# Optimization experiments

Measured on AMD Instinct MI355X. Metric: run time of the kernel, lower is better.

## Reference

```python
import jax, jax.numpy as jnp
import numpy as np

D_MODEL = 1024
NUM_HEADS = 16
HEAD_DIM = D_MODEL // NUM_HEADS  # 64
ROPE_THETA = 10000.0
BATCH = 2
SEQ = 2048
NEG_INF = -1e30


def setup_inputs() -> dict:
    key = jax.random.key(0)
    ks = jax.random.split(key, 6)
    std = 1.0 / np.sqrt(D_MODEL)
    x = jax.random.normal(ks[0], (BATCH, SEQ, D_MODEL), dtype=jnp.float32)
    wq = jax.random.normal(ks[1], (D_MODEL, D_MODEL), dtype=jnp.float32) * std
    wk = jax.random.normal(ks[2], (D_MODEL, D_MODEL), dtype=jnp.float32) * std
    wv = jax.random.normal(ks[3], (D_MODEL, D_MODEL), dtype=jnp.float32) * std
    wo = jax.random.normal(ks[4], (D_MODEL, D_MODEL), dtype=jnp.float32) * std
    token_positions = jnp.broadcast_to(jnp.arange(SEQ, dtype=jnp.int32)[None, :], (BATCH, SEQ))
    return {"x": x, "token_positions": token_positions, "wq": wq, "wk": wk, "wv": wv, "wo": wo}


def _apply_rope(t, token_positions):
    # t: (B, H, S, head_dim), token_positions: (B, S)
    half = HEAD_DIM // 2
    inv_freq = 1.0 / (ROPE_THETA ** (2.0 * jnp.arange(half, dtype=jnp.float32) / HEAD_DIM))
    angles = token_positions.astype(jnp.float32)[..., None] * inv_freq  # (B, S, half)
    cos = jnp.cos(angles)[:, None, :, :]  # (B, 1, S, half)
    sin = jnp.sin(angles)[:, None, :, :]
    tp = t.reshape(*t.shape[:-1], half, 2)  # interleaved pairs
    x1, x2 = tp[..., 0], tp[..., 1]
    r1 = x1 * cos - x2 * sin
    r2 = x1 * sin + x2 * cos
    return jnp.stack([r1, r2], axis=-1).reshape(t.shape)


def reference(x, token_positions, wq, wk, wv, wo):
    B, S, D = x.shape
    H, hd = NUM_HEADS, HEAD_DIM
    # projections (Linear: y = x @ W.T, no bias)
    q = (x @ wq.T).reshape(B, S, H, hd).transpose(0, 2, 1, 3)  # (B, H, S, hd)
    k = (x @ wk.T).reshape(B, S, H, hd).transpose(0, 2, 1, 3)
    v = (x @ wv.T).reshape(B, S, H, hd).transpose(0, 2, 1, 3)
    # RoPE on Q, K
    q = _apply_rope(q, token_positions)
    k = _apply_rope(k, token_positions)
    # causal scaled dot-product attention
    scores = jnp.einsum("bhqd,bhkd->bhqk", q, k) / jnp.sqrt(jnp.float32(hd))
    mask = jnp.tril(jnp.ones((S, S), dtype=bool))
    scores = jnp.where(mask, scores, NEG_INF)
    probs = jax.nn.softmax(scores, axis=-1)
    attn = jnp.einsum("bhqk,bhkd->bhqd", probs, v)  # (B, H, S, hd)
    attn = attn.transpose(0, 2, 1, 3).reshape(B, S, D)
    return attn @ wo.T
```

## Files before the change

### kernel.cpp

```cpp
#include <hip/hip_runtime.h>
#include <stdint.h>
#include <math.h>

#define SEQ 2048
#define NH 16
#define DM 1024

typedef __bf16 bf16x8 __attribute__((ext_vector_type(8)));
typedef __bf16 bf16x2 __attribute__((ext_vector_type(2)));
typedef short s16x4 __attribute__((ext_vector_type(4)));
typedef short s16x8 __attribute__((ext_vector_type(8)));
typedef float f32x4 __attribute__((ext_vector_type(4)));
typedef float f32x2 __attribute__((ext_vector_type(2)));

#define ASM_VMCNT0  asm volatile("s_waitcnt vmcnt(0)" ::: "memory")
#define ASM_BARRIER asm volatile("s_barrier" ::: "memory")

__device__ __forceinline__ unsigned short f2bf(float f) {
  union { float f; unsigned u; } v; v.f = f;
  unsigned r = v.u + 0x7fffu + ((v.u >> 16) & 1u);
  return (unsigned short)(r >> 16);
}
__device__ __forceinline__ unsigned pk2(float a, float b) {
  f32x2 v = {a, b};
  bf16x2 r = __builtin_convertvector(v, bf16x2);
  union { bf16x2 h; unsigned u; } c; c.h = r;
  return c.u;
}
__device__ __forceinline__ void load_lds16(const void* g, void* l) {
  __builtin_amdgcn_global_load_lds((__attribute__((address_space(1))) void*)g,
                                   (__attribute__((address_space(3))) void*)l,
                                   16, 0, 0);
}

__global__ void cvt_all(const float* __restrict__ x, const float* __restrict__ wq,
                        const float* __restrict__ wk, const float* __restrict__ wv,
                        const float* __restrict__ wo, unsigned short* __restrict__ ws) {
  const int i = blockIdx.x * blockDim.x + threadIdx.x;
  const int off = i * 4;
  const float* src;
  unsigned short* dst;
  if (off < 4194304) {
    src = x + off;  dst = ws + off;
  } else {
    const int r = off - 4194304;
    const int w = r >> 20, o = r & 1048575;
    const float* tabs[4] = {wq, wk, wv, wo};
    src = tabs[w] + o;  dst = ws + 4194304 + (w << 20) + o;
  }
  const float4 v = *(const float4*)src;
  uint2 u;
  u.x = pk2(v.x, v.y);
  u.y = pk2(v.z, v.w);
  *(uint2*)dst = u;
}

__launch_bounds__(256, 3)
__global__ void gemm_qkv(const unsigned short* __restrict__ X,
                         const unsigned short* __restrict__ W3,
                         unsigned short* __restrict__ Qr,
                         unsigned short* __restrict__ Kr,
                         unsigned short* __restrict__ Vt,
                         const int* __restrict__ tp) {
  __shared__ __align__(16) char smem[32768];

  const int t = threadIdx.x;
  const int lane = t & 63, wave = t >> 6;
  const int quad = lane >> 4, l16 = lane & 15;
  const int m0 = blockIdx.y * 128, n0 = blockIdx.x * 128;
  const int wm = (wave >> 1) * 64, wn = (wave & 1) * 64;

  f32x4 acc[4][4];
#pragma unroll
  for (int i = 0; i < 4; i++)
#pragma unroll
    for (int j = 0; j < 4; j++) { acc[i][j][0]=0.f; acc[i][j][1]=0.f; acc[i][j][2]=0.f; acc[i][j][3]=0.f; }

  const int rr = t >> 2;
  const int cc = (t & 3) * 8;

#define QKV_STAGE(bufidx, k0_) do {                                               \
    char* a_ = smem + (bufidx) * 8192;                                            \
    char* b_ = smem + 16384 + (bufidx) * 8192;                                    \
    _Pragma("unroll")                                                             \
    for (int i_ = 0; i_ < 2; i_++) {                                              \
      load_lds16(X  + (uint64_t)(m0 + i_ * 64 + rr) * 1024 + (k0_) + cc,          \
                 a_ + i_ * 4096 + wave * 1024);                                   \
      load_lds16(W3 + (uint64_t)(n0 + i_ * 64 + rr) * 1024 + (k0_) + cc,          \
                 b_ + i_ * 4096 + wave * 1024);                                   \
    }                                                                             \
  } while (0)

  QKV_STAGE(0, 0);

  for (int k0 = 0; k0 < 1024; k0 += 32) {
    const int buf = (k0 >> 5) & 1;
    ASM_VMCNT0;
    ASM_BARRIER;
    if (k0 + 32 < 1024) QKV_STAGE(buf ^ 1, k0 + 32);
    char* As = smem + buf * 8192;
    char* Bs = smem + 16384 + buf * 8192;

    bf16x8 af[4], bfr[4];
#pragma unroll
    for (int i = 0; i < 4; i++) {
      af[i]  = *(const bf16x8*)(As + (wm + i * 16 + l16) * 64 + quad * 16);
      bfr[i] = *(const bf16x8*)(Bs + (wn + i * 16 + l16) * 64 + quad * 16);
    }
#pragma unroll
    for (int i = 0; i < 4; i++)
#pragma unroll
      for (int j = 0; j < 4; j++)
        acc[i][j] = __builtin_amdgcn_mfma_f32_16x16x32_bf16(af[i], bfr[j], acc[i][j], 0, 0, 0);
  }
#undef QKV_STAGE

  if (n0 < 2048) {
    unsigned short* dst = (n0 < 1024) ? Qr : Kr;
    float fr[4]; int dd[4], hh[4];
#pragma unroll
    for (int j = 0; j < 4; j++) {
      const int n = n0 + wn + j * 16 + l16;
      dd[j] = n & 63;
      hh[j] = (n & 1023) >> 6;
      fr[j] = __builtin_amdgcn_exp2f(-0.20762050594f * (float)(dd[j] & ~1)) * 0.15915494309f;
    }
    const float sgnodd = (l16 & 1) ? 1.f : -1.f;
#pragma unroll
    for (int i = 0; i < 4; i++) {
#pragma unroll
      for (int r = 0; r < 4; r++) {
        const int m = m0 + wm + i * 16 + quad * 4 + r;
        const int s = m & 2047, b = m >> 11;
        const float posf = (float)tp[m];
#pragma unroll
        for (int j = 0; j < 4; j++) {
          const float v = acc[i][j][r];
          const float p = __shfl_xor(v, 1);
          float rev = posf * fr[j];
          rev -= floorf(rev);
          float sn, cs;
          asm("v_sin_f32 %0, %1" : "=v"(sn) : "v"(rev));
          asm("v_cos_f32 %0, %1" : "=v"(cs) : "v"(rev));
          const float rv = fmaf(v, cs, p * sn * sgnodd);
          dst[((uint64_t)((b * NH + hh[j]) * SEQ + s)) * 64 + dd[j]] = f2bf(rv);
        }
      }
    }
  } else {
#pragma unroll
    for (int i = 0; i < 4; i++) {
      const int m = m0 + wm + i * 16 + quad * 4;
      const int s = m & 2047, b = m >> 11;
      const int sl = s & 63;
      const int qv = (sl >> 2) & 3, nv = sl >> 4;
      const int g = (s & ~63) + qv * 16 + (nv >> 1) * 8 + (nv & 1) * 4;
#pragma unroll
      for (int j = 0; j < 4; j++) {
        const int n = n0 - 2048 + wn + j * 16 + l16;
        const int h = n >> 6, d = n & 63;
        uint2 w;
        w.x = pk2(acc[i][j][0], acc[i][j][1]);
        w.y = pk2(acc[i][j][2], acc[i][j][3]);
        *(uint2*)(Vt + ((uint64_t)((b * NH + h) * 64 + d)) * SEQ + g) = w;
      }
    }
  }
}

__launch_bounds__(512, 2)
__global__ void gemm_ao(const unsigned short* __restrict__ A,
                        const unsigned short* __restrict__ B,
                        float* __restrict__ C) {
  __shared__ __align__(16) char smem[32768];

  const int t = threadIdx.x;
  const int lane = t & 63, wave = t >> 6;
  const int quad = lane >> 4, l16 = lane & 15;
  const int id = blockIdx.y * 8 + blockIdx.x;
  const int k = id & 7;
  const int tt = id >> 3;
  const int m0 = (k * 4 + (tt & 3)) * 128;
  const int n0 = (tt >> 2) * 128;
  const int wm = (wave >> 2) * 64;
  const int wn = (wave & 3) * 32;

  f32x4 acc[4][2];
#pragma unroll
  for (int i = 0; i < 4; i++)
#pragma unroll
    for (int j = 0; j < 2; j++) { acc[i][j][0]=0.f; acc[i][j][1]=0.f; acc[i][j][2]=0.f; acc[i][j][3]=0.f; }

  const int rr = t >> 2;
  const int cc = (t & 3) * 8;

#define AO_STAGE(bufidx, k0_) do {                                               \
    char* a_ = smem + (bufidx) * 8192;                                            \
    char* b_ = smem + 16384 + (bufidx) * 8192;                                    \
    load_lds16(A + (uint64_t)(m0 + rr) * 1024 + (k0_) + cc, a_ + wave * 1024);    \
    load_lds16(B + (uint64_t)(n0 + rr) * 1024 + (k0_) + cc, b_ + wave * 1024);    \
  } while (0)

  AO_STAGE(0, 0);

  for (int k0 = 0; k0 < 1024; k0 += 32) {
    const int buf = (k0 >> 5) & 1;
    ASM_VMCNT0;
    ASM_BARRIER;
    if (k0 + 32 < 1024) AO_STAGE(buf ^ 1, k0 + 32);
    char* As = smem + buf * 8192;
    char* Bs = smem + 16384 + buf * 8192;

    bf16x8 af[4], bfr[2];
#pragma unroll
    for (int i = 0; i < 4; i++)
      af[i]  = *(const bf16x8*)(As + (wm + i * 16 + l16) * 64 + quad * 16);
#pragma unroll
    for (int j = 0; j < 2; j++)
      bfr[j] = *(const bf16x8*)(Bs + (wn + j * 16 + l16) * 64 + quad * 16);
#pragma unroll
    for (int i = 0; i < 4; i++)
#pragma unroll
      for (int j = 0; j < 2; j++)
        acc[i][j] = __builtin_amdgcn_mfma_f32_16x16x32_bf16(af[i], bfr[j], acc[i][j], 0, 0, 0);
  }
#undef AO_STAGE

#pragma unroll
  for (int i = 0; i < 4; i++)
#pragma unroll
    for (int j = 0; j < 2; j++)
#pragma unroll
      for (int r = 0; r < 4; r++) {
        const int m = m0 + wm + i * 16 + quad * 4 + r;
        const int n = n0 + wn + j * 16 + l16;
        C[(uint64_t)m * DM + n] = acc[i][j][r];
      }
}

__launch_bounds__(256, 4)
__global__ void flash_attn(const unsigned short* __restrict__ Q,
                           const unsigned short* __restrict__ K,
                           const unsigned short* __restrict__ Vt,
                           unsigned short* __restrict__ Oa) {
  __shared__ __align__(16) char smem[32768];

  const int t = threadIdx.x;
  const int lane = t & 63, wid = t >> 6;
  const int quad = lane >> 4, l16 = lane & 15;
  const int u = blockIdx.x;
  const int m = u >> 5;
  const int tq = (m < 16) ? (31 - m) : (m - 16);
  const int bh = u & 31;
  const uint64_t base = (uint64_t)bh * (SEQ * 64);
  const int qb = tq * 64;
  const int ng = tq + 1;
  const int qg = qb + wid * 16 + l16;
  const int b = bh >> 4, h = bh & 15;

  bf16x8 qf[2];
  {
    const unsigned short* qp = Q + base + (uint64_t)qg * 64 + quad * 8;
    qf[0] = *(const bf16x8*)qp;  qf[1] = *(const bf16x8*)(qp + 32);
  }

  f32x4 o[4];
#pragma unroll
  for (int i = 0; i < 4; i++) { o[i][0]=0.f; o[i][1]=0.f; o[i][2]=0.f; o[i][3]=0.f; }
  float lI = 0.f;

  const int sr8 = lane >> 3;
  const int sc = ((lane & 7) ^ sr8) * 8;
  const int swz = (l16 & 7);

#define STAGE(bufidx, kb_) do {                                                   \
    _Pragma("unroll")                                                             \
    for (int i_ = 0; i_ < 2; i_++) {                                              \
      const int r_ = wid * 16 + i_ * 8 + sr8;                                     \
      load_lds16(K  + base + (uint64_t)((kb_) + r_) * 64 + sc,                    \
                 smem + (bufidx) * 8192 + wid * 2048 + i_ * 1024);                \
      load_lds16(Vt + base + (uint64_t)r_ * SEQ + (kb_) + sc,                     \
                 smem + 16384 + (bufidx) * 8192 + wid * 2048 + i_ * 1024);        \
    }                                                                             \
  } while (0)

  STAGE(0, 0);

  const float c1 = 0.18033688011f;

  for (int it = 0; it < ng; it++) {
    const int kb = it * 64;
    const int buf = it & 1;
    ASM_VMCNT0;
    ASM_BARRIER;
    if (it + 1 < ng) STAGE(buf ^ 1, (it + 1) * 64);
    char* ks = smem + buf * 8192;
    char* vs = smem + 16384 + buf * 8192;

    int nbmax = ((qb + wid * 16 + 15 - kb) >> 4) + 1;
    nbmax = nbmax > 4 ? 4 : (nbmax < 0 ? 0 : nbmax);
    const bool diag = (kb + 63) > (qb + wid * 16);

    f32x4 sf[4];
    float ls = 0.f;
#pragma unroll
    for (int nb = 0; nb < 4; nb++) {
      if (nb < nbmax) {
        f32x4 s; s[0]=0.f; s[1]=0.f; s[2]=0.f; s[3]=0.f;
#pragma unroll
        for (int kk = 0; kk < 2; kk++) {
          bf16x8 kfr = *(const bf16x8*)(ks + (nb * 16 + l16) * 128 + (((kk * 4 + quad) ^ swz) * 16));
          s = __builtin_amdgcn_mfma_f32_16x16x32_bf16(kfr, qf[kk], s, 0, 0, 0);
        }
        if (diag) {
#pragma unroll
          for (int r = 0; r < 4; r++) {
            const int key = kb + nb * 16 + quad * 4 + r;
            const float p = (key <= qg) ? __builtin_amdgcn_exp2f(s[r] * c1) : 0.f;
            sf[nb][r] = p;  ls += p;
          }
        } else {
#pragma unroll
          for (int r = 0; r < 4; r++) {
            const float p = __builtin_amdgcn_exp2f(s[r] * c1);
            sf[nb][r] = p;  ls += p;
          }
        }
      }
    }
    lI += ls;

#pragma unroll
    for (int np = 0; np < 2; np++) {
      if (2 * np < nbmax) {
        union { uint2 u; s16x4 h; } p0;
        p0.u.x = pk2(sf[2 * np][0], sf[2 * np][1]);
        p0.u.y = pk2(sf[2 * np][2], sf[2 * np][3]);
        const bool hi = (2 * np + 1 < nbmax);
        union { uint2 u; s16x4 h; } p1;
        if (hi) {
          p1.u.x = pk2(sf[2 * np + 1][0], sf[2 * np + 1][1]);
          p1.u.y = pk2(sf[2 * np + 1][2], sf[2 * np + 1][3]);
        }
#pragma unroll
        for (int db = 0; db < 4; db++) {
          s16x8 vv = *(const s16x8*)(vs + (db * 16 + l16) * 128 +
                                     (((quad * 2 + np) ^ swz) * 16));
          s16x4 vlo = __builtin_shufflevector(vv, vv, 0, 1, 2, 3);
          o[db] = __builtin_amdgcn_mfma_f32_16x16x16bf16_1k(vlo, p0.h, o[db], 0, 0, 0);
          if (hi) {
            s16x4 vhi = __builtin_shufflevector(vv, vv, 4, 5, 6, 7);
            o[db] = __builtin_amdgcn_mfma_f32_16x16x16bf16_1k(vhi, p1.h, o[db], 0, 0, 0);
          }
        }
      }
    }
  }
#undef STAGE

  float lr = lI;
  lr += __shfl_xor(lr, 16);
  lr += __shfl_xor(lr, 32);
  const float invl = 1.0f / lr;
  unsigned short* orow = Oa + ((uint64_t)(b * SEQ + qg)) * DM + h * 64 + quad * 4;
#pragma unroll
  for (int db = 0; db < 4; db++) {
    uint2 w;
    w.x = pk2(o[db][0] * invl, o[db][1] * invl);
    w.y = pk2(o[db][2] * invl, o[db][3] * invl);
    *(uint2*)(orow + db * 16) = w;
  }
}

extern "C" void kernel_launch(void* const* d_in, const int* in_sizes, int n_in,
                              void* d_out, int out_size, void* d_ws, size_t ws_size,
                              hipStream_t stream) {
  const float* x  = (const float*)d_in[0];
  const int* tp   = (const int*)d_in[1];
  const float* wq = (const float*)d_in[2];
  const float* wk = (const float*)d_in[3];
  const float* wv = (const float*)d_in[4];
  const float* wo = (const float*)d_in[5];
  float* out = (float*)d_out;

  unsigned short* ws = (unsigned short*)d_ws;
  unsigned short* xb  = ws;
  unsigned short* w3b = ws + 4194304;
  unsigned short* wob = ws + 7340032;
  unsigned short* Qr  = ws + 8388608;
  unsigned short* Kr  = ws + 12582912;
  unsigned short* Vt  = ws + 16777216;
  unsigned short* At  = ws + 20971520;

  cvt_all<<<8192, 256, 0, stream>>>(x, wq, wk, wv, wo, ws);
  gemm_qkv<<<dim3(24, 32), 256, 0, stream>>>(xb, w3b, Qr, Kr, Vt, tp);
  flash_attn<<<1024, 256, 0, stream>>>(Qr, Kr, Vt, At);
  gemm_ao<<<dim3(8, 32), 512, 0, stream>>>(At, wob, out);
}
```

Baseline: 171.0 us.

## Split flash-attention work across waves by key halves with LDS reduction

Each wave now owns 32 query rows and one half of each 64-key tile, instead of 16 query rows and the full key tile. Each K and V fragment read from LDS is reused for two query sub-blocks, and diagonal masking work is spread more evenly across waves. Partial outputs and row sums from the two key-half waves are combined through shared memory at the end. This costs extra accumulator registers, an LDS reduction pass and two more barriers.

Result: faster. 165.7 us, median of 3 (-3.1%).

```diff
diff --git a/kernel.cpp b/kernel.cpp
--- a/kernel.cpp
+++ b/kernel.cpp
@@ -14,6 +14,7 @@
 typedef float f32x2 __attribute__((ext_vector_type(2)));
 
 #define ASM_VMCNT0  asm volatile("s_waitcnt vmcnt(0)" ::: "memory")
+#define ASM_LGKM0   asm volatile("s_waitcnt lgkmcnt(0)" ::: "memory")
 #define ASM_BARRIER asm volatile("s_barrier" ::: "memory")
 
 __device__ __forceinline__ unsigned short f2bf(float f) {
@@ -248,6 +249,8 @@
   const int t = threadIdx.x;
   const int lane = t & 63, wid = t >> 6;
   const int quad = lane >> 4, l16 = lane & 15;
+  const int kw = wid & 1;
+  const int qw = wid >> 1;
   const int u = blockIdx.x;
   const int m = u >> 5;
   const int tq = (m < 16) ? (31 - m) : (m - 16);
@@ -255,19 +258,23 @@
   const uint64_t base = (uint64_t)bh * (SEQ * 64);
   const int qb = tq * 64;
   const int ng = tq + 1;
-  const int qg = qb + wid * 16 + l16;
   const int b = bh >> 4, h = bh & 15;
-
-  bf16x8 qf[2];
+  const int qlo = qb + qw * 32;
+
+  bf16x8 qf[2][2];
   {
-    const unsigned short* qp = Q + base + (uint64_t)qg * 64 + quad * 8;
-    qf[0] = *(const bf16x8*)qp;  qf[1] = *(const bf16x8*)(qp + 32);
-  }
-
-  f32x4 o[4];
-#pragma unroll
-  for (int i = 0; i < 4; i++) { o[i][0]=0.f; o[i][1]=0.f; o[i][2]=0.f; o[i][3]=0.f; }
-  float lI = 0.f;
+    const unsigned short* qp0 = Q + base + (uint64_t)(qlo + l16) * 64 + quad * 8;
+    qf[0][0] = *(const bf16x8*)qp0;  qf[0][1] = *(const bf16x8*)(qp0 + 32);
+    const unsigned short* qp1 = Q + base + (uint64_t)(qlo + 16 + l16) * 64 + quad * 8;
+    qf[1][0] = *(const bf16x8*)qp1;  qf[1][1] = *(const bf16x8*)(qp1 + 32);
+  }
+
+  f32x4 o[2][4];
+#pragma unroll
+  for (int qg = 0; qg < 2; qg++)
+#pragma unroll
+    for (int db = 0; db < 4; db++) { o[qg][db][0]=0.f; o[qg][db][1]=0.f; o[qg][db][2]=0.f; o[qg][db][3]=0.f; }
+  float lI0 = 0.f, lI1 = 0.f;
 
   const int sr8 = lane >> 3;
   const int sc = ((lane & 7) ^ sr8) * 8;
@@ -297,78 +304,108 @@
     char* ks = smem + buf * 8192;
     char* vs = smem + 16384 + buf * 8192;
 
-    int nbmax = ((qb + wid * 16 + 15 - kb) >> 4) + 1;
-    nbmax = nbmax > 4 ? 4 : (nbmax < 0 ? 0 : nbmax);
-    const bool diag = (kb + 63) > (qb + wid * 16);
-
-    f32x4 sf[4];
-    float ls = 0.f;
-#pragma unroll
-    for (int nb = 0; nb < 4; nb++) {
-      if (nb < nbmax) {
-        f32x4 s; s[0]=0.f; s[1]=0.f; s[2]=0.f; s[3]=0.f;
-#pragma unroll
-        for (int kk = 0; kk < 2; kk++) {
-          bf16x8 kfr = *(const bf16x8*)(ks + (nb * 16 + l16) * 128 + (((kk * 4 + quad) ^ swz) * 16));
-          s = __builtin_amdgcn_mfma_f32_16x16x32_bf16(kfr, qf[kk], s, 0, 0, 0);
-        }
-        if (diag) {
-#pragma unroll
-          for (int r = 0; r < 4; r++) {
-            const int key = kb + nb * 16 + quad * 4 + r;
-            const float p = (key <= qg) ? __builtin_amdgcn_exp2f(s[r] * c1) : 0.f;
-            sf[nb][r] = p;  ls += p;
+    int nv = ((qlo + 31 - kb) >> 4) + 1 - 2 * kw;
+    nv = nv > 2 ? 2 : (nv < 0 ? 0 : nv);
+    const bool diag = (kb + kw * 32 + 31) > qlo;
+
+    if (nv > 0) {
+      f32x4 sf0[2], sf1[2];
+      float ls0 = 0.f, ls1 = 0.f;
+#pragma unroll
+      for (int nbp = 0; nbp < 2; nbp++) {
+        if (nbp < nv) {
+          f32x4 s0; s0[0]=0.f; s0[1]=0.f; s0[2]=0.f; s0[3]=0.f;
+          f32x4 s1; s1[0]=0.f; s1[1]=0.f; s1[2]=0.f; s1[3]=0.f;
+#pragma unroll
+          for (int kk = 0; kk < 2; kk++) {
+            bf16x8 kfr = *(const bf16x8*)(ks + ((2 * kw + nbp) * 16 + l16) * 128 +
+                                          (((kk * 4 + quad) ^ swz) * 16));
+            s0 = __builtin_amdgcn_mfma_f32_16x16x32_bf16(kfr, qf[0][kk], s0, 0, 0, 0);
+            s1 = __builtin_amdgcn_mfma_f32_16x16x32_bf16(kfr, qf[1][kk], s1, 0, 0, 0);
           }
-        } else {
-#pragma unroll
-          for (int r = 0; r < 4; r++) {
-            const float p = __builtin_amdgcn_exp2f(s[r] * c1);
-            sf[nb][r] = p;  ls += p;
+          if (diag) {
+#pragma unroll
+            for (int r = 0; r < 4; r++) {
+              const int key = kb + (2 * kw + nbp) * 16 + quad * 4 + r;
+              const float p0 = (key <= qlo + l16)      ? __builtin_amdgcn_exp2f(s0[r] * c1) : 0.f;
+              const float p1 = (key <= qlo + 16 + l16) ? __builtin_amdgcn_exp2f(s1[r] * c1) : 0.f;
+              sf0[nbp][r] = p0;  ls0 += p0;
+              sf1[nbp][r] = p1;  ls1 += p1;
+            }
+          } else {
+#pragma unroll
+            for (int r = 0; r < 4; r++) {
+              const float p0 = __builtin_amdgcn_exp2f(s0[r] * c1);
+              const float p1 = __builtin_amdgcn_exp2f(s1[r] * c1);
+              sf0[nbp][r] = p0;  ls0 += p0;
+              sf1[nbp][r] = p1;  ls1 += p1;
+            }
           }
         }
       }
-    }
-    lI += ls;
-
-#pragma unroll
-    for (int np = 0; np < 2; np++) {
-      if (2 * np < nbmax) {
-        union { uint2 u; s16x4 h; } p0;
-        p0.u.x = pk2(sf[2 * np][0], sf[2 * np][1]);
-        p0.u.y = pk2(sf[2 * np][2], sf[2 * np][3]);
-        const bool hi = (2 * np + 1 < nbmax);
-        union { uint2 u; s16x4 h; } p1;
+      lI0 += ls0;  lI1 += ls1;
+
+      union { uint2 u; s16x4 h; } a0, b0, a1, b1;
+      a0.u.x = pk2(sf0[0][0], sf0[0][1]);  a0.u.y = pk2(sf0[0][2], sf0[0][3]);
+      b0.u.x = pk2(sf1[0][0], sf1[0][1]);  b0.u.y = pk2(sf1[0][2], sf1[0][3]);
+      const bool hi = (nv > 1);
+      if (hi) {
+        a1.u.x = pk2(sf0[1][0], sf0[1][1]);  a1.u.y = pk2(sf0[1][2], sf0[1][3]);
+        b1.u.x = pk2(sf1[1][0], sf1[1][1]);  b1.u.y = pk2(sf1[1][2], sf1[1][3]);
+      }
+#pragma unroll
+      for (int db = 0; db < 4; db++) {
+        s16x8 vv = *(const s16x8*)(vs + (db * 16 + l16) * 128 +
+                                   (((quad * 2 + kw) ^ swz) * 16));
+        s16x4 vlo = __builtin_shufflevector(vv, vv, 0, 1, 2, 3);
+        o[0][db] = __builtin_amdgcn_mfma_f32_16x16x16bf16_1k(vlo, a0.h, o[0][db], 0, 0, 0);
+        o[1][db] = __builtin_amdgcn_mfma_f32_16x16x16bf16_1k(vlo, b0.h, o[1][db], 0, 0, 0);
         if (hi) {
-          p1.u.x = pk2(sf[2 * np + 1][0], sf[2 * np + 1][1]);
-          p1.u.y = pk2(sf[2 * np + 1][2], sf[2 * np + 1][3]);
+          s16x4 vhi = __builtin_shufflevector(vv, vv, 4, 5, 6, 7);
+          o[0][db] = __builtin_amdgcn_mfma_f32_16x16x16bf16_1k(vhi, a1.h, o[0][db], 0, 0, 0);
+          o[1][db] = __builtin_amdgcn_mfma_f32_16x16x16bf16_1k(vhi, b1.h, o[1][db], 0, 0, 0);
         }
-#pragma unroll
-        for (int db = 0; db < 4; db++) {
-          s16x8 vv = *(const s16x8*)(vs + (db * 16 + l16) * 128 +
-                                     (((quad * 2 + np) ^ swz) * 16));
-          s16x4 vlo = __builtin_shufflevector(vv, vv, 0, 1, 2, 3);
-          o[db] = __builtin_amdgcn_mfma_f32_16x16x16bf16_1k(vlo, p0.h, o[db], 0, 0, 0);
-          if (hi) {
-            s16x4 vhi = __builtin_shufflevector(vv, vv, 4, 5, 6, 7);
-            o[db] = __builtin_amdgcn_mfma_f32_16x16x16bf16_1k(vhi, p1.h, o[db], 0, 0, 0);
-          }
-        }
       }
     }
   }
 #undef STAGE
 
-  float lr = lI;
-  lr += __shfl_xor(lr, 16);
-  lr += __shfl_xor(lr, 32);
-  const float invl = 1.0f / lr;
-  unsigned short* orow = Oa + ((uint64_t)(b * SEQ + qg)) * DM + h * 64 + quad * 4;
-#pragma unroll
-  for (int db = 0; db < 4; db++) {
-    uint2 w;
-    w.x = pk2(o[db][0] * invl, o[db][1] * invl);
-    w.y = pk2(o[db][2] * invl, o[db][3] * invl);
-    *(uint2*)(orow + db * 16) = w;
+  float lr0 = lI0;  lr0 += __shfl_xor(lr0, 16);  lr0 += __shfl_xor(lr0, 32);
+  float lr1 = lI1;  lr1 += __shfl_xor(lr1, 16);  lr1 += __shfl_xor(lr1, 32);
+
+  ASM_LGKM0;
+  ASM_BARRIER;
+  if (kw) {
+    char* pbase = smem + qw * 8192;
+#pragma unroll
+    for (int qg = 0; qg < 2; qg++)
+#pragma unroll
+      for (int db = 0; db < 4; db++)
+        *(f32x4*)(pbase + (qg * 4 + db) * 1024 + quad * 256 + l16 * 16) = o[qg][db];
+    if (quad == 0) {
+      *(float*)(smem + 16384 + qw * 128 + l16 * 4) = lr0;
+      *(float*)(smem + 16384 + qw * 128 + 64 + l16 * 4) = lr1;
+    }
+  }
+  ASM_LGKM0;
+  ASM_BARRIER;
+  if (!kw) {
+    char* pbase = smem + qw * 8192;
+#pragma unroll
+    for (int qg = 0; qg < 2; qg++) {
+      const float lpart = *(const float*)(smem + 16384 + qw * 128 + qg * 64 + l16 * 4);
+      const float invl = 1.0f / ((qg ? lr1 : lr0) + lpart);
+      const int qrow = qlo + qg * 16 + l16;
+      unsigned short* orow = Oa + ((uint64_t)(b * SEQ + qrow)) * DM + h * 64 + quad * 4;
+#pragma unroll
+      for (int db = 0; db < 4; db++) {
+        const f32x4 p = *(const f32x4*)(pbase + (qg * 4 + db) * 1024 + quad * 256 + l16 * 16);
+        uint2 w;
+        w.x = pk2((o[qg][db][0] + p[0]) * invl, (o[qg][db][1] + p[1]) * invl);
+        w.y = pk2((o[qg][db][2] + p[2]) * invl, (o[qg][db][3] + p[3]) * invl);
+        *(uint2*)(orow + db * 16) = w;
+      }
+    }
   }
 }
 
```
